# Performance work log

Hardware: AMD Instinct MI355X
Metric: run time of the kernel (lower is better)

Reference implementation:

```python
import jax, jax.numpy as jnp
import numpy as np

K_FRAC = 0.5  # matches init kwarg k


def setup_inputs() -> dict:
    key = jax.random.key(0)
    g = jax.random.normal(key, (16, 2048, 2048), dtype=jnp.float32)
    return {"g": g}


def reference(g):
    # k = int(N * k_frac): number of SMALLEST entries per row to zero out
    N = g.shape[-1]
    k = int(N * K_FRAC)
    g2 = g.reshape(-1, N)                       # [R, N]
    # indices of the k smallest values per row (topk of -g)
    _, idx = jax.lax.top_k(-g2, k)              # [R, k] int32
    rows = jnp.arange(g2.shape[0])[:, None]     # [R, 1]
    t = g2.at[rows, idx].set(0.0)               # scatter zeros at bottom-k positions
    return t.reshape(g.shape)
```

## Files before the change

kernel.cpp:

```cpp
#include <hip/hip_runtime.h>

#define ROW_N 2048
#define ROW_K 1024
#define NSUB 4
#define HPAD 264
#define WH   (NSUB * HPAD)
#define WSTRIDE (WH + 4)

__device__ __forceinline__ void wfence() {
    asm volatile("s_waitcnt lgkmcnt(0)" ::: "memory");
}

__device__ __forceinline__ unsigned f2key(float x) {
    unsigned u = __float_as_uint(x);
    return u ^ ((unsigned)((int)u >> 31) | 0x80000000u);
}
__device__ __forceinline__ float key2f(unsigned k) {
    unsigned u = (k & 0x80000000u) ? (k ^ 0x80000000u) : ~k;
    return __uint_as_float(u);
}

__device__ __forceinline__ void scan_pick(unsigned b0, unsigned b1, unsigned b2,
                                          unsigned b3, int lane, int rank_in,
                                          unsigned& digit, int& rank_out,
                                          int& cnteq_out) {
    unsigned s4 = b0 + b1 + b2 + b3;
    unsigned incl = s4;
#pragma unroll
    for (int off = 1; off < 64; off <<= 1) {
        unsigned n = __shfl_up(incl, off, 64);
        if (lane >= off) incl += n;
    }
    int excl = (int)(incl - s4);
    bool found = (rank_in >= excl) && (rank_in < (int)incl);
    int rr = rank_in - excl;
    unsigned d = 4 * lane;
    unsigned beq = b0;
    if (found) {
        if (rr >= (int)b0) { rr -= (int)b0; d++; beq = b1;
            if (rr >= (int)b1) { rr -= (int)b1; d++; beq = b2;
                if (rr >= (int)b2) { rr -= (int)b2; d++; beq = b3; } } }
    }
    unsigned pack = (d << 24) | (beq << 12) | (unsigned)rr;
    unsigned long long bal = __ballot(found);
    int src = __builtin_ctzll(bal);
    pack = (unsigned)__shfl((int)pack, src, 64);
    digit = pack >> 24;
    cnteq_out = (int)((pack >> 12) & 0xfffu);
    rank_out = (int)(pack & 0xfffu);
}

__global__ __launch_bounds__(256, 8)
void ktakes_kernel(const float* __restrict__ g, float* __restrict__ out) {
    const int tid  = threadIdx.x;
    const int wave = tid >> 6;
    const int lane = tid & 63;
    const int row  = blockIdx.x * 4 + wave;

    __shared__ unsigned H[4 * WSTRIDE];
    unsigned* hw   = H + wave * WSTRIDE;
    uint4*    hw4  = reinterpret_cast<uint4*>(hw);
    unsigned* hsub = hw + (lane & (NSUB - 1)) * HPAD;

    const float4* g4 = reinterpret_cast<const float4*>(g + (size_t)row * ROW_N);
    float4*       o4 = reinterpret_cast<float4*>(out + (size_t)row * ROW_N);

    unsigned k[32];
#pragma unroll
    for (int j = 0; j < 8; ++j) {
        float4 v = g4[j * 64 + lane];
        k[4*j+0] = f2key(v.x); k[4*j+1] = f2key(v.y);
        k[4*j+2] = f2key(v.z); k[4*j+3] = f2key(v.w);
    }

    const uint4 z4 = {0u, 0u, 0u, 0u};
    unsigned prefix;
    int rank, cnteq;

    {
#pragma unroll
        for (int i = 0; i < 4; ++i) hw4[i * 64 + lane] = z4;
        if (lane < 32) hw[1024 + lane] = 0;
        wfence();
#pragma unroll
        for (int c = 0; c < 32; ++c)
            atomicAdd(&hsub[k[c] >> 24], 1u);
        wfence();
        unsigned b0 = 0, b1 = 0, b2 = 0, b3 = 0;
#pragma unroll
        for (int s = 0; s < NSUB; ++s) {
            uint4 h = *reinterpret_cast<const uint4*>(&hw[s * HPAD + 4 * lane]);
            b0 += h.x; b1 += h.y; b2 += h.z; b3 += h.w;
        }
        wfence();
        unsigned d;
        scan_pick(b0, b1, b2, b3, lane, ROW_K - 1, d, rank, cnteq);
        prefix = d << 24;
    }

#pragma unroll
    for (int r = 1; r < 4; ++r) {
        const int shift = 24 - 8 * r;
        const int hs = shift + 8;

        hw4[lane] = z4;
        wfence();
#pragma unroll
        for (int c = 0; c < 32; ++c)
            if (((k[c] ^ prefix) >> hs) == 0)
                atomicAdd(&hw[(k[c] >> shift) & 255u], 1u);
        wfence();
        uint4 h = hw4[lane];
        wfence();
        unsigned d;
        scan_pick(h.x, h.y, h.z, h.w, lane, rank, d, rank, cnteq);
        prefix |= d << shift;
    }

    const unsigned Kth = prefix;
    const int m = rank + 1;

    unsigned zm = 0;
    if (cnteq == m) {
#pragma unroll
        for (int c = 0; c < 32; ++c)
            if (k[c] <= Kth) zm |= 1u << c;
    } else {
        int base = 0;
#pragma unroll
        for (int j = 0; j < 8; ++j) {
            int eqmask = 0, e = 0;
#pragma unroll
            for (int c = 0; c < 4; ++c) {
                bool q = (k[4*j+c] == Kth);
                eqmask |= (int)q << c; e += (int)q;
            }
            int incl = e;
#pragma unroll
            for (int off = 1; off < 64; off <<= 1) {
                int n = __shfl_up(incl, off, 64);
                if (lane >= off) incl += n;
            }
            int excl = incl - e;
            int tot = __shfl(incl, 63, 64);
            int pos = base + excl;
#pragma unroll
            for (int c = 0; c < 4; ++c) {
                if (eqmask & (1 << c)) {
                    if (pos < m) zm |= 1u << (4*j+c);
                    pos++;
                }
            }
            base += tot;
        }
#pragma unroll
        for (int c = 0; c < 32; ++c)
            if (k[c] < Kth) zm |= 1u << c;
    }

#pragma unroll
    for (int j = 0; j < 8; ++j) {
        float4 v;
        v.x = (zm >> (4*j+0)) & 1u ? 0.0f : key2f(k[4*j+0]);
        v.y = (zm >> (4*j+1)) & 1u ? 0.0f : key2f(k[4*j+1]);
        v.z = (zm >> (4*j+2)) & 1u ? 0.0f : key2f(k[4*j+2]);
        v.w = (zm >> (4*j+3)) & 1u ? 0.0f : key2f(k[4*j+3]);
        o4[j * 64 + lane] = v;
    }
}

extern "C" void kernel_launch(void* const* d_in, const int* in_sizes, int n_in,
                              void* d_out, int out_size, void* d_ws, size_t ws_size,
                              hipStream_t stream) {
    const float* g = (const float*)d_in[0];
    float* out = (float*)d_out;
    const int rows = in_sizes[0] / ROW_N;
    hipLaunchKernelGGL(ktakes_kernel, dim3(rows / 4), dim3(256), 0, stream, g, out);
}
```

Before: 450.2 us.

## Use DPP wave scan, double-buffered histograms, fewer sub-histograms in radix select

```diff
diff --git a/kernel.cpp b/kernel.cpp
--- a/kernel.cpp
+++ b/kernel.cpp
@@ -2,10 +2,11 @@
 
 #define ROW_N 2048
 #define ROW_K 1024
-#define NSUB 4
-#define HPAD 264
-#define WH   (NSUB * HPAD)
-#define WSTRIDE (WH + 4)
+#define HPAD  264
+#define BUFA  528
+#define BUFB  784
+#define WHTOT 1040
+#define WSTRIDE 1048
 
 __device__ __forceinline__ void wfence() {
     asm volatile("s_waitcnt lgkmcnt(0)" ::: "memory");
@@ -20,17 +21,23 @@
     return __uint_as_float(u);
 }
 
+__device__ __forceinline__ unsigned wave_incl_scan(unsigned x) {
+    int v = (int)x;
+    v += __builtin_amdgcn_update_dpp(0, v, 0x111, 0xf, 0xf, false);
+    v += __builtin_amdgcn_update_dpp(0, v, 0x112, 0xf, 0xf, false);
+    v += __builtin_amdgcn_update_dpp(0, v, 0x114, 0xf, 0xf, false);
+    v += __builtin_amdgcn_update_dpp(0, v, 0x118, 0xf, 0xf, false);
+    v += __builtin_amdgcn_update_dpp(0, v, 0x142, 0xa, 0xf, false);
+    v += __builtin_amdgcn_update_dpp(0, v, 0x143, 0xc, 0xf, false);
+    return (unsigned)v;
+}
+
 __device__ __forceinline__ void scan_pick(unsigned b0, unsigned b1, unsigned b2,
                                           unsigned b3, int lane, int rank_in,
                                           unsigned& digit, int& rank_out,
                                           int& cnteq_out) {
     unsigned s4 = b0 + b1 + b2 + b3;
-    unsigned incl = s4;
-#pragma unroll
-    for (int off = 1; off < 64; off <<= 1) {
-        unsigned n = __shfl_up(incl, off, 64);
-        if (lane >= off) incl += n;
-    }
+    unsigned incl = wave_incl_scan(s4);
     int excl = (int)(incl - s4);
     bool found = (rank_in >= excl) && (rank_in < (int)incl);
     int rr = rank_in - excl;
@@ -43,14 +50,14 @@
     }
     unsigned pack = (d << 24) | (beq << 12) | (unsigned)rr;
     unsigned long long bal = __ballot(found);
-    int src = __builtin_ctzll(bal);
-    pack = (unsigned)__shfl((int)pack, src, 64);
+    int src = (int)__builtin_ctzll(bal);
+    pack = (unsigned)__builtin_amdgcn_readlane((int)pack, src);
     digit = pack >> 24;
     cnteq_out = (int)((pack >> 12) & 0xfffu);
     rank_out = (int)(pack & 0xfffu);
 }
 
-__global__ __launch_bounds__(256, 8)
+__global__ __launch_bounds__(256)
 void ktakes_kernel(const float* __restrict__ g, float* __restrict__ out) {
     const int tid  = threadIdx.x;
     const int wave = tid >> 6;
@@ -60,10 +67,15 @@
     __shared__ unsigned H[4 * WSTRIDE];
     unsigned* hw   = H + wave * WSTRIDE;
     uint4*    hw4  = reinterpret_cast<uint4*>(hw);
-    unsigned* hsub = hw + (lane & (NSUB - 1)) * HPAD;
+    unsigned* hsub = hw + (lane & 1) * HPAD;
 
     const float4* g4 = reinterpret_cast<const float4*>(g + (size_t)row * ROW_N);
     float4*       o4 = reinterpret_cast<float4*>(out + (size_t)row * ROW_N);
+
+    const uint4 z4 = {0u, 0u, 0u, 0u};
+#pragma unroll
+    for (int i = 0; i < 4; ++i) hw4[i * 64 + lane] = z4;
+    if (lane < 16) hw[1024 + lane] = 0;
 
     unsigned k[32];
 #pragma unroll
@@ -73,48 +85,55 @@
         k[4*j+2] = f2key(v.z); k[4*j+3] = f2key(v.w);
     }
 
-    const uint4 z4 = {0u, 0u, 0u, 0u};
     unsigned prefix;
     int rank, cnteq;
+    unsigned d;
 
+    wfence();
+#pragma unroll
+    for (int c = 0; c < 32; ++c)
+        atomicAdd(&hsub[k[c] >> 24], 1u);
+    wfence();
     {
-#pragma unroll
-        for (int i = 0; i < 4; ++i) hw4[i * 64 + lane] = z4;
-        if (lane < 32) hw[1024 + lane] = 0;
-        wfence();
-#pragma unroll
-        for (int c = 0; c < 32; ++c)
-            atomicAdd(&hsub[k[c] >> 24], 1u);
-        wfence();
-        unsigned b0 = 0, b1 = 0, b2 = 0, b3 = 0;
-#pragma unroll
-        for (int s = 0; s < NSUB; ++s) {
-            uint4 h = *reinterpret_cast<const uint4*>(&hw[s * HPAD + 4 * lane]);
-            b0 += h.x; b1 += h.y; b2 += h.z; b3 += h.w;
-        }
-        wfence();
-        unsigned d;
-        scan_pick(b0, b1, b2, b3, lane, ROW_K - 1, d, rank, cnteq);
+        uint4 h0 = *reinterpret_cast<const uint4*>(&hw[4 * lane]);
+        uint4 h1 = *reinterpret_cast<const uint4*>(&hw[HPAD + 4 * lane]);
+        scan_pick(h0.x + h1.x, h0.y + h1.y, h0.z + h1.z, h0.w + h1.w,
+                  lane, ROW_K - 1, d, rank, cnteq);
         prefix = d << 24;
     }
 
 #pragma unroll
-    for (int r = 1; r < 4; ++r) {
-        const int shift = 24 - 8 * r;
-        const int hs = shift + 8;
+    for (int c = 0; c < 32; ++c)
+        if (((k[c] ^ prefix) >> 24) == 0)
+            atomicAdd(&hw[BUFA + ((k[c] >> 16) & 255u)], 1u);
+    wfence();
+    {
+        uint4 h = *reinterpret_cast<const uint4*>(&hw[BUFA + 4 * lane]);
+        scan_pick(h.x, h.y, h.z, h.w, lane, rank, d, rank, cnteq);
+        prefix |= d << 16;
+    }
 
-        hw4[lane] = z4;
-        wfence();
 #pragma unroll
-        for (int c = 0; c < 32; ++c)
-            if (((k[c] ^ prefix) >> hs) == 0)
-                atomicAdd(&hw[(k[c] >> shift) & 255u], 1u);
-        wfence();
-        uint4 h = hw4[lane];
-        wfence();
-        unsigned d;
+    for (int c = 0; c < 32; ++c)
+        if (((k[c] ^ prefix) >> 16) == 0)
+            atomicAdd(&hw[BUFB + ((k[c] >> 8) & 255u)], 1u);
+    *reinterpret_cast<uint4*>(&hw[BUFA + 4 * lane]) = z4;
+    wfence();
+    {
+        uint4 h = *reinterpret_cast<const uint4*>(&hw[BUFB + 4 * lane]);
         scan_pick(h.x, h.y, h.z, h.w, lane, rank, d, rank, cnteq);
-        prefix |= d << shift;
+        prefix |= d << 8;
+    }
+
+#pragma unroll
+    for (int c = 0; c < 32; ++c)
+        if (((k[c] ^ prefix) >> 8) == 0)
+            atomicAdd(&hw[BUFA + (k[c] & 255u)], 1u);
+    wfence();
+    {
+        uint4 h = *reinterpret_cast<const uint4*>(&hw[BUFA + 4 * lane]);
+        scan_pick(h.x, h.y, h.z, h.w, lane, rank, d, rank, cnteq);
+        prefix |= d;
     }
 
     const unsigned Kth = prefix;
```

Result: faster. 430.5 us (-4.4%).
